# Performance work log

Hardware: AMD Instinct MI355X
Metric: run time of the kernel (lower is better)

The kernel has to match this reference:

```python
import jax, jax.numpy as jnp
import numpy as np

B, S, D = 4, 2048, 1024
H = 16
KD = 1024  # key_dim (total)
VD = 1024  # value_dim (total)


def setup_inputs() -> dict:
    key = jax.random.key(0)
    ks = jax.random.split(key, 8)
    queries = jax.random.normal(ks[0], (B, S, D), dtype=jnp.float32)
    keys_ = jax.random.normal(ks[1], (B, S, D), dtype=jnp.float32)
    values = jax.random.normal(ks[2], (B, S, D), dtype=jnp.float32)
    # causal float mask (1 = keep, 0 = masked), broadcasts over [B, H, S, S]
    mask = jnp.tril(jnp.ones((S, S), dtype=jnp.float32))[None, None]
    # Linear weights stored as [in, out] so forward is x @ W
    Wq = jax.random.normal(ks[3], (D, KD), dtype=jnp.float32) / np.sqrt(D)
    Wk = jax.random.normal(ks[4], (D, KD), dtype=jnp.float32) / np.sqrt(D)
    Wv = jax.random.normal(ks[5], (D, VD), dtype=jnp.float32) / np.sqrt(D)
    Wo = jax.random.normal(ks[6], (H * VD // H * H // H * 1 if False else VD, D), dtype=jnp.float32) / np.sqrt(VD)
    bo = jnp.zeros((D,), dtype=jnp.float32)
    return {"queries": queries, "keys": keys_, "values": values, "mask": mask,
            "Wq": Wq, "Wk": Wk, "Wv": Wv, "Wo": Wo, "bo": bo}


def reference(queries, keys, values, mask, Wq, Wk, Wv, Wo, bo):
    b, s, _ = queries.shape
    # project then split heads: [B, S, H, hd] -> [B, H, S, hd]
    q = (queries @ Wq).reshape(b, s, H, -1).transpose(0, 2, 1, 3)
    k = (keys @ Wk).reshape(b, s, H, -1).transpose(0, 2, 1, 3)
    v = (values @ Wv).reshape(b, s, H, -1).transpose(0, 2, 1, 3)
    dk = k.shape[-1]  # per-head key dim (scale uses post-split dk, as in source)
    logits = jnp.einsum('bhqd,bhkd->bhqk', q, k) / jnp.sqrt(jnp.float32(dk))
    logits = logits + (1.0 - mask) * (-1e9)
    attn = jax.nn.softmax(logits, axis=-1)  # dropout p=0 in eval -> identity
    o = jnp.einsum('bhqk,bhkd->bhqd', attn, v)
    o = o.transpose(0, 2, 1, 3).reshape(b, s, H * (VD // H))
    return o @ Wo + bo
```

## Files before the change

kernel.cpp:

```cpp
#include <hip/hip_runtime.h>
#include <hip/hip_bf16.h>

typedef __attribute__((ext_vector_type(8))) short s8v;
typedef __attribute__((ext_vector_type(4))) short s4v;
typedef __attribute__((ext_vector_type(4))) float f4v;

#define S_LEN 2048
#define NH 16
#define HD 64
#define DMODEL 1024
#define KVB 64
#define LOG2E 1.44269504088896f
#define FIXMAX 32.0f

__device__ __forceinline__ unsigned short f2bf(float f) {
  union { float f; unsigned int u; } v; v.f = f;
  return (unsigned short)((v.u + 0x7FFFu + ((v.u >> 16) & 1u)) >> 16);
}

__device__ __forceinline__ f4v mfma16(s8v a, s8v b, f4v c) {
  return __builtin_amdgcn_mfma_f32_16x16x32_bf16(a, b, c, 0, 0, 0);
}

__device__ __forceinline__ void gl_lds16(const unsigned short* g, unsigned short* l) {
  __builtin_amdgcn_global_load_lds(
      (const __attribute__((address_space(1))) void*)g,
      (__attribute__((address_space(3))) void*)l, 16, 0, 0);
}

__global__ __launch_bounds__(256)
void transpose_cast4(const float* __restrict__ w0, const float* __restrict__ w1,
                     const float* __restrict__ w2, const float* __restrict__ w3,
                     unsigned short* __restrict__ o0, unsigned short* __restrict__ o1,
                     unsigned short* __restrict__ o2, unsigned short* __restrict__ o3) {
  __shared__ float tile[32][33];
  const int z = blockIdx.z;
  const float* W = (z == 0) ? w0 : (z == 1) ? w1 : (z == 2) ? w2 : w3;
  unsigned short* Wt = (z == 0) ? o0 : (z == 1) ? o1 : (z == 2) ? o2 : o3;
  int x = threadIdx.x, y = threadIdx.y;
  int n0 = blockIdx.x * 32, k0 = blockIdx.y * 32;
#pragma unroll
  for (int i = 0; i < 32; i += 8)
    tile[y + i][x] = W[(size_t)(k0 + y + i) * DMODEL + n0 + x];
  __syncthreads();
#pragma unroll
  for (int i = 0; i < 32; i += 8)
    Wt[(size_t)(n0 + y + i) * DMODEL + k0 + x] = f2bf(tile[x][y + i]);
}

__global__ __launch_bounds__(256, 2)
void qkv_gemm(const float* __restrict__ Qf, const float* __restrict__ Kf,
              const float* __restrict__ Vf, const unsigned short* __restrict__ WqT,
              const unsigned short* __restrict__ WkT, const unsigned short* __restrict__ WvT,
              unsigned short* __restrict__ Qb, unsigned short* __restrict__ Kb,
              unsigned short* __restrict__ Vtb) {
  __shared__ unsigned short As[128 * 64];
  __shared__ unsigned short Bs[128 * 64];
  const int z = blockIdx.z;
  const float* Af = (z == 0) ? Qf : (z == 1) ? Kf : Vf;
  const unsigned short* Bt = (z == 0) ? WqT : (z == 1) ? WkT : WvT;
  unsigned short* C = (z == 0) ? Qb : (z == 1) ? Kb : Vtb;
  const float scale = (z == 0) ? 0.125f * LOG2E : 1.0f;

  const int t = threadIdx.x;
  const int l = t & 63;
  const int w = t >> 6, wr = w >> 1, wc = w & 1;
  const int m0 = blockIdx.x * 128, n0 = blockIdx.y * 128;
  const int lg = l >> 4, lm = l & 15;

  f4v acc[4][4];
#pragma unroll
  for (int i = 0; i < 4; i++)
#pragma unroll
    for (int j = 0; j < 4; j++) acc[i][j] = f4v{0.f, 0.f, 0.f, 0.f};

  const int lr = l >> 3;
  const int sj = l & 7;
  const float* Arow = Af + (size_t)(m0 + w * 8 + lr) * DMODEL + sj * 8;
  const unsigned short* Bprow =
      Bt + (size_t)(n0 + w * 8 + lr) * DMODEL + (sj ^ lr) * 8;
  const int xo0 = (lg ^ (lm & 7)) << 4;
  const int xo1 = ((4 + lg) ^ (lm & 7)) << 4;

  for (int k0 = 0; k0 < DMODEL; k0 += 64) {
#pragma unroll
    for (int i = 0; i < 4; i++)
      gl_lds16(Bprow + (size_t)(i * 32) * DMODEL + k0, &Bs[i * 2048 + w * 512]);
#pragma unroll
    for (int i = 0; i < 4; i++) {
      const float* src = Arow + (size_t)(i * 32) * DMODEL + k0;
      f4v v0 = *(const f4v*)src;
      f4v v1 = *(const f4v*)(src + 4);
      unsigned int u0, u1, u2, u3;
      asm("v_cvt_pk_bf16_f32 %0, %1, %2" : "=v"(u0) : "v"(v0[0]), "v"(v0[1]));
      asm("v_cvt_pk_bf16_f32 %0, %1, %2" : "=v"(u1) : "v"(v0[2]), "v"(v0[3]));
      asm("v_cvt_pk_bf16_f32 %0, %1, %2" : "=v"(u2) : "v"(v1[0]), "v"(v1[1]));
      asm("v_cvt_pk_bf16_f32 %0, %1, %2" : "=v"(u3) : "v"(v1[2]), "v"(v1[3]));
      uint4 pk; pk.x = u0; pk.y = u1; pk.z = u2; pk.w = u3;
      *(uint4*)((char*)As + (i * 32 + w * 8 + lr) * 128 + (sj ^ lr) * 16) = pk;
    }
    __syncthreads();

    s8v af[4][2], bf[4][2];
#pragma unroll
    for (int mi = 0; mi < 4; mi++) {
      const char* ar = (const char*)As + (wr * 64 + mi * 16 + lm) * 128;
      af[mi][0] = *(const s8v*)(ar + xo0);
      af[mi][1] = *(const s8v*)(ar + xo1);
    }
#pragma unroll
    for (int ni = 0; ni < 4; ni++) {
      const char* br = (const char*)Bs + (wc * 64 + ni * 16 + lm) * 128;
      bf[ni][0] = *(const s8v*)(br + xo0);
      bf[ni][1] = *(const s8v*)(br + xo1);
    }
#pragma unroll
    for (int mi = 0; mi < 4; mi++)
#pragma unroll
      for (int ni = 0; ni < 4; ni++) {
        acc[mi][ni] = mfma16(af[mi][0], bf[ni][0], acc[mi][ni]);
        acc[mi][ni] = mfma16(af[mi][1], bf[ni][1], acc[mi][ni]);
      }
    __syncthreads();
  }

#pragma unroll
  for (int mi = 0; mi < 4; mi++)
#pragma unroll
    for (int ni = 0; ni < 4; ni++) {
      int col = n0 + wc * 64 + ni * 16 + lm;
#pragma unroll
      for (int rr = 0; rr < 4; rr++) {
        int row = m0 + wr * 64 + mi * 16 + lg * 4 + rr;
        unsigned short h = f2bf(acc[mi][ni][rr] * scale);
        int b = row >> 11, s = row & 2047, hh = col >> 6, d = col & 63;
        if (z < 2)
          C[(((size_t)(b * NH + hh)) * S_LEN + s) * HD + d] = h;
        else
          C[(((size_t)(b * NH + hh)) * HD + d) * S_LEN + s] = h;
      }
    }
}

__global__ __launch_bounds__(256, 2)
void out_gemm(const unsigned short* __restrict__ A, const unsigned short* __restrict__ Bt,
              float* __restrict__ Cp, const float* __restrict__ bias) {
  __shared__ unsigned short As[128 * 64];
  __shared__ unsigned short Bs[128 * 64];
  const int t = threadIdx.x;
  const int l = t & 63;
  const int w = t >> 6, wr = w >> 1, wc = w & 1;
  const int m0 = blockIdx.x * 128, n0 = blockIdx.y * 128;
  const int lg = l >> 4, lm = l & 15;

  f4v acc[4][4];
#pragma unroll
  for (int i = 0; i < 4; i++)
#pragma unroll
    for (int j = 0; j < 4; j++) acc[i][j] = f4v{0.f, 0.f, 0.f, 0.f};

  const int sgc = (l & 7) ^ ((l >> 3) & 7);
  const unsigned short* Aprow = A + (size_t)(m0 + w * 8 + (l >> 3)) * DMODEL + sgc * 8;
  const unsigned short* Bprow = Bt + (size_t)(n0 + w * 8 + (l >> 3)) * DMODEL + sgc * 8;
  const int xo0 = (lg ^ (lm & 7)) << 4;
  const int xo1 = ((4 + lg) ^ (lm & 7)) << 4;

  for (int k0 = 0; k0 < DMODEL; k0 += 64) {
#pragma unroll
    for (int i = 0; i < 4; i++) {
      gl_lds16(Aprow + (size_t)(i * 32) * DMODEL + k0, &As[i * 2048 + w * 512]);
      gl_lds16(Bprow + (size_t)(i * 32) * DMODEL + k0, &Bs[i * 2048 + w * 512]);
    }
    __syncthreads();

    s8v af[4][2], bf[4][2];
#pragma unroll
    for (int mi = 0; mi < 4; mi++) {
      const char* ar = (const char*)As + (wr * 64 + mi * 16 + lm) * 128;
      af[mi][0] = *(const s8v*)(ar + xo0);
      af[mi][1] = *(const s8v*)(ar + xo1);
    }
#pragma unroll
    for (int ni = 0; ni < 4; ni++) {
      const char* br = (const char*)Bs + (wc * 64 + ni * 16 + lm) * 128;
      bf[ni][0] = *(const s8v*)(br + xo0);
      bf[ni][1] = *(const s8v*)(br + xo1);
    }
#pragma unroll
    for (int mi = 0; mi < 4; mi++)
#pragma unroll
      for (int ni = 0; ni < 4; ni++) {
        acc[mi][ni] = mfma16(af[mi][0], bf[ni][0], acc[mi][ni]);
        acc[mi][ni] = mfma16(af[mi][1], bf[ni][1], acc[mi][ni]);
      }
    __syncthreads();
  }

#pragma unroll
  for (int mi = 0; mi < 4; mi++)
#pragma unroll
    for (int ni = 0; ni < 4; ni++) {
      int col = n0 + wc * 64 + ni * 16 + lm;
      float bv = bias[col];
#pragma unroll
      for (int rr = 0; rr < 4; rr++) {
        int row = m0 + wr * 64 + mi * 16 + lg * 4 + rr;
        Cp[(size_t)row * DMODEL + col] = acc[mi][ni][rr] + bv;
      }
    }
}

__global__ __launch_bounds__(256, 2)
void attn_k(const unsigned short* __restrict__ Q, const unsigned short* __restrict__ Km,
            const unsigned short* __restrict__ Vt, unsigned short* __restrict__ O) {
  __shared__ unsigned short Ks[2][KVB * HD];
  __shared__ unsigned short Vs[2][HD * KVB];
  __shared__ unsigned short pbuf[16][16 * KVB];
  const int t = threadIdx.x, l = t & 63, w = t >> 6;
  const int lg = l >> 4, lm = l & 15;

  const int c = blockIdx.x;
  const int bh = c & 63;
  const int pr4 = (c >> 6) & 3;
  const int pr = (c >> 8) ? 7 - pr4 : pr4;
  const int s0A = (15 - pr) * 128, s0B = pr * 128;

  const unsigned short* Qh = Q + (size_t)bh * S_LEN * HD;
  const unsigned short* Kh = Km + (size_t)bh * S_LEN * HD;
  const unsigned short* Vh = Vt + (size_t)bh * HD * S_LEN;

  const int xo0 = (lg ^ (lm & 7)) << 4;
  const int xo1 = ((4 + lg) ^ (lm & 7)) << 4;

  const int q00 = s0A + w * 32, q01 = q00 + 16;
  const int q02 = s0B + w * 32, q03 = q02 + 16;

  s8v qf0[2], qf1[2], qf2[2], qf3[2];
#define LOADQ(QF, Q0)                                                   \
  QF[0] = *(const s8v*)(Qh + (size_t)((Q0) + lm) * HD + lg * 8);        \
  QF[1] = *(const s8v*)(Qh + (size_t)((Q0) + lm) * HD + 32 + lg * 8);
  LOADQ(qf0, q00) LOADQ(qf1, q01) LOADQ(qf2, q02) LOADQ(qf3, q03)
#undef LOADQ

  f4v o0[4], o1[4], o2[4], o3[4];
#pragma unroll
  for (int i = 0; i < 4; i++) {
    o0[i] = f4v{0.f, 0.f, 0.f, 0.f}; o1[i] = f4v{0.f, 0.f, 0.f, 0.f};
    o2[i] = f4v{0.f, 0.f, 0.f, 0.f}; o3[i] = f4v{0.f, 0.f, 0.f, 0.f};
  }
  float l0_ = 0.f, l1_ = 0.f, l2_ = 0.f, l3_ = 0.f;

  const int sr0 = w * 8 + (l >> 3);
  const int sj = l & 7;

#define STAGE(buf, kv)                                                          \
  {                                                                             \
    _Pragma("unroll")                                                           \
    for (int i = 0; i < 2; i++) {                                               \
      int r_ = sr0 + i * 32;                                                    \
      int jj_ = ((sj ^ (r_ & 7)) << 3);                                         \
      gl_lds16(Kh + (size_t)((kv) + r_) * HD + jj_, &Ks[buf][w * 512 + i * 2048]); \
      gl_lds16(Vh + (size_t)r_ * S_LEN + (kv) + jj_, &Vs[buf][w * 512 + i * 2048]); \
    }                                                                           \
  }

#define TILE_S(QF, LL, Q0, PI)                                                  \
  {                                                                             \
    const int dt = (Q0) >> 6;                                                   \
    if (ti <= dt) {                                                             \
      f4v s_[4];                                                                \
      __builtin_amdgcn_s_setprio(1);                                            \
      _Pragma("unroll")                                                         \
      for (int sub = 0; sub < 4; sub++) {                                       \
        s_[sub] = f4v{0.f, 0.f, 0.f, 0.f};                                      \
        s_[sub] = mfma16(kf[sub * 2], QF[0], s_[sub]);                          \
        s_[sub] = mfma16(kf[sub * 2 + 1], QF[1], s_[sub]);                      \
      }                                                                         \
      __builtin_amdgcn_s_setprio(0);                                            \
      if (ti == dt) {                                                           \
        const int qrow = (Q0) + lm;                                             \
        _Pragma("unroll")                                                       \
        for (int sub = 0; sub < 4; sub++) {                                     \
          const int kbase = kv + sub * 16 + lg * 4;                             \
          _Pragma("unroll")                                                     \
          for (int rr = 0; rr < 4; rr++)                                        \
            if (kbase + rr > qrow) s_[sub][rr] = -1e30f;                        \
        }                                                                       \
      }                                                                         \
      char* pb_ = (char*)pbuf[w * 4 + PI];                                      \
      float psum = 0.f;                                                         \
      _Pragma("unroll")                                                         \
      for (int sub = 0; sub < 4; sub++) {                                       \
        float p0 = exp2f(s_[sub][0] - FIXMAX);                                  \
        float p1 = exp2f(s_[sub][1] - FIXMAX);                                  \
        float p2 = exp2f(s_[sub][2] - FIXMAX);                                  \
        float p3 = exp2f(s_[sub][3] - FIXMAX);                                  \
        psum += (p0 + p1) + (p2 + p3);                                          \
        unsigned int u01, u23;                                                  \
        asm("v_cvt_pk_bf16_f32 %0, %1, %2" : "=v"(u01) : "v"(p0), "v"(p1));     \
        asm("v_cvt_pk_bf16_f32 %0, %1, %2" : "=v"(u23) : "v"(p2), "v"(p3));     \
        const int cc = (sub * 4 + lg) ^ ((lm & 7) << 1);                        \
        uint2 pv; pv.x = u01; pv.y = u23;                                       \
        *(uint2*)(pb_ + lm * 128 + (cc << 3)) = pv;                             \
      }                                                                         \
      (LL) += psum;                                                             \
    }                                                                           \
  }

#define TILE_PV(OO, Q0, PI)                                                     \
  {                                                                             \
    const int dt = (Q0) >> 6;                                                   \
    if (ti <= dt) {                                                             \
      const char* pb_ = (const char*)pbuf[w * 4 + PI];                          \
      s8v pf0 = *(const s8v*)(pb_ + lm * 128 + xo0);                            \
      s8v pf1 = *(const s8v*)(pb_ + lm * 128 + xo1);                            \
      __builtin_amdgcn_s_setprio(1);                                            \
      _Pragma("unroll")                                                         \
      for (int nc = 0; nc < 4; nc++) {                                          \
        OO[nc] = mfma16(vf[nc * 2], pf0, OO[nc]);                               \
        OO[nc] = mfma16(vf[nc * 2 + 1], pf1, OO[nc]);                           \
      }                                                                         \
      __builtin_amdgcn_s_setprio(0);                                            \
    }                                                                           \
  }

  const int nt = 2 * (15 - pr) + 2;
  int cur = 0;
  STAGE(0, 0);
  __syncthreads();

  for (int ti = 0; ti < nt; ++ti) {
    const int kv = ti * 64;
    if (ti + 1 < nt) STAGE(cur ^ 1, kv + 64);

    const unsigned short* Kb = Ks[cur];
    const unsigned short* Vb = Vs[cur];

    s8v kf[8];
#pragma unroll
    for (int sub = 0; sub < 4; sub++) {
      const char* krow = (const char*)Kb + (sub * 16 + lm) * 128;
      kf[sub * 2] = *(const s8v*)(krow + xo0);
      kf[sub * 2 + 1] = *(const s8v*)(krow + xo1);
    }

    TILE_S(qf0, l0_, q00, 0);
    TILE_S(qf1, l1_, q01, 1);
    TILE_S(qf2, l2_, q02, 2);
    TILE_S(qf3, l3_, q03, 3);

    __builtin_amdgcn_sched_barrier(0);

    s8v vf[8];
#pragma unroll
    for (int sub = 0; sub < 4; sub++) {
      const char* vrow = (const char*)Vb + (sub * 16 + lm) * 128;
      vf[sub * 2] = *(const s8v*)(vrow + xo0);
      vf[sub * 2 + 1] = *(const s8v*)(vrow + xo1);
    }

    TILE_PV(o0, q00, 0);
    TILE_PV(o1, q01, 1);
    TILE_PV(o2, q02, 2);
    TILE_PV(o3, q03, 3);

    __syncthreads();
    cur ^= 1;
  }

  const int b = bh >> 4, hh = bh & 15;
#define EPI(OO, LL, Q0)                                                         \
  {                                                                             \
    float lt = (LL);                                                            \
    lt += __shfl_xor(lt, 16);                                                   \
    lt += __shfl_xor(lt, 32);                                                   \
    const float inv = 1.f / lt;                                                 \
    unsigned short* Orow =                                                      \
        O + ((size_t)b * S_LEN + (Q0) + lm) * DMODEL + hh * HD;                 \
    _Pragma("unroll")                                                           \
    for (int nc = 0; nc < 4; nc++) {                                            \
      unsigned short h4[4];                                                     \
      _Pragma("unroll")                                                         \
      for (int rr = 0; rr < 4; rr++) h4[rr] = f2bf(OO[nc][rr] * inv);           \
      *(s4v*)(Orow + nc * 16 + lg * 4) = *(const s4v*)h4;                       \
    }                                                                           \
  }
  EPI(o0, l0_, q00);
  EPI(o1, l1_, q01);
  EPI(o2, l2_, q02);
  EPI(o3, l3_, q03);
#undef EPI
#undef TILE_PV
#undef TILE_S
#undef STAGE
}

extern "C" void kernel_launch(void* const* d_in, const int* in_sizes, int n_in,
                              void* d_out, int out_size, void* d_ws, size_t ws_size,
                              hipStream_t stream) {
  const float* queries = (const float*)d_in[0];
  const float* keys = (const float*)d_in[1];
  const float* values = (const float*)d_in[2];
  const float* Wq = (const float*)d_in[4];
  const float* Wk = (const float*)d_in[5];
  const float* Wv = (const float*)d_in[6];
  const float* Wo = (const float*)d_in[7];
  const float* bo = (const float*)d_in[8];

  char* ws = (char*)d_ws;
  const size_t WB = (size_t)DMODEL * DMODEL * 2;
  unsigned short* WqT = (unsigned short*)(ws + 0 * WB);
  unsigned short* WkT = (unsigned short*)(ws + 1 * WB);
  unsigned short* WvT = (unsigned short*)(ws + 2 * WB);
  unsigned short* WoT = (unsigned short*)(ws + 3 * WB);
  const size_t TB = (size_t)4 * S_LEN * DMODEL * 2;
  unsigned short* Qb  = (unsigned short*)(ws + 4 * WB);
  unsigned short* Kb  = (unsigned short*)(ws + 4 * WB + TB);
  unsigned short* Vtb = (unsigned short*)(ws + 4 * WB + 2 * TB);
  unsigned short* Ob  = (unsigned short*)(ws + 4 * WB + 3 * TB);

  const int M = 4 * S_LEN;

  transpose_cast4<<<dim3(32, 32, 4), dim3(32, 8), 0, stream>>>(
      Wq, Wk, Wv, Wo, WqT, WkT, WvT, WoT);

  qkv_gemm<<<dim3(64, 8, 3), 256, 0, stream>>>(queries, keys, values,
                                               WqT, WkT, WvT, Qb, Kb, Vtb);

  attn_k<<<512, 256, 0, stream>>>(Qb, Kb, Vtb, Ob);

  out_gemm<<<dim3(64, 8), 256, 0, stream>>>(Ob, WoT, (float*)d_out, bo);
}
```

Measured before the change: 176.9 us.

## Double-buffer LDS tiles in QKV projection GEMM to overlap loads with MFMA

Doubles the shared-memory A and B tiles in the QKV projection GEMM. The next k-slice is loaded (async B copy plus A fp32-to-bf16 convert and store) while the current slice is read and fed to MFMA, leaving one barrier per iteration instead of two. This hides global-load latency behind compute. In exchange, LDS use doubles to 64KB per block, which may lower occupancy against the launch bound of 2 blocks per CU.

Result: slower. 201.7 us (+14.0%).

```diff
diff --git a/kernel.cpp b/kernel.cpp
--- a/kernel.cpp
+++ b/kernel.cpp
@@ -54,8 +54,8 @@
               const unsigned short* __restrict__ WkT, const unsigned short* __restrict__ WvT,
               unsigned short* __restrict__ Qb, unsigned short* __restrict__ Kb,
               unsigned short* __restrict__ Vtb) {
-  __shared__ unsigned short As[128 * 64];
-  __shared__ unsigned short Bs[128 * 64];
+  __shared__ unsigned short As[2][128 * 64];
+  __shared__ unsigned short Bs[2][128 * 64];
   const int z = blockIdx.z;
   const float* Af = (z == 0) ? Qf : (z == 1) ? Kf : Vf;
   const unsigned short* Bt = (z == 0) ? WqT : (z == 1) ? WkT : WvT;
@@ -82,38 +82,55 @@
   const int xo0 = (lg ^ (lm & 7)) << 4;
   const int xo1 = ((4 + lg) ^ (lm & 7)) << 4;
 
+#define STAGE_A(bb, kk)                                                         \
+  {                                                                             \
+    _Pragma("unroll")                                                           \
+    for (int i = 0; i < 4; i++) {                                               \
+      const float* src = Arow + (size_t)(i * 32) * DMODEL + (kk);               \
+      f4v v0 = *(const f4v*)src;                                                \
+      f4v v1 = *(const f4v*)(src + 4);                                          \
+      unsigned int u0, u1, u2, u3;                                              \
+      asm("v_cvt_pk_bf16_f32 %0, %1, %2" : "=v"(u0) : "v"(v0[0]), "v"(v0[1]));  \
+      asm("v_cvt_pk_bf16_f32 %0, %1, %2" : "=v"(u1) : "v"(v0[2]), "v"(v0[3]));  \
+      asm("v_cvt_pk_bf16_f32 %0, %1, %2" : "=v"(u2) : "v"(v1[0]), "v"(v1[1]));  \
+      asm("v_cvt_pk_bf16_f32 %0, %1, %2" : "=v"(u3) : "v"(v1[2]), "v"(v1[3]));  \
+      uint4 pk; pk.x = u0; pk.y = u1; pk.z = u2; pk.w = u3;                     \
+      *(uint4*)((char*)As[bb] + (i * 32 + w * 8 + lr) * 128 + (sj ^ lr) * 16) = pk; \
+    }                                                                           \
+  }
+#define STAGE_B(bb, kk)                                                         \
+  {                                                                             \
+    _Pragma("unroll")                                                           \
+    for (int i = 0; i < 4; i++)                                                 \
+      gl_lds16(Bprow + (size_t)(i * 32) * DMODEL + (kk),                        \
+               &Bs[bb][i * 2048 + w * 512]);                                    \
+  }
+
+  STAGE_B(0, 0);
+  STAGE_A(0, 0);
+  __syncthreads();
+  int cur = 0;
+
   for (int k0 = 0; k0 < DMODEL; k0 += 64) {
-#pragma unroll
-    for (int i = 0; i < 4; i++)
-      gl_lds16(Bprow + (size_t)(i * 32) * DMODEL + k0, &Bs[i * 2048 + w * 512]);
-#pragma unroll
-    for (int i = 0; i < 4; i++) {
-      const float* src = Arow + (size_t)(i * 32) * DMODEL + k0;
-      f4v v0 = *(const f4v*)src;
-      f4v v1 = *(const f4v*)(src + 4);
-      unsigned int u0, u1, u2, u3;
-      asm("v_cvt_pk_bf16_f32 %0, %1, %2" : "=v"(u0) : "v"(v0[0]), "v"(v0[1]));
-      asm("v_cvt_pk_bf16_f32 %0, %1, %2" : "=v"(u1) : "v"(v0[2]), "v"(v0[3]));
-      asm("v_cvt_pk_bf16_f32 %0, %1, %2" : "=v"(u2) : "v"(v1[0]), "v"(v1[1]));
-      asm("v_cvt_pk_bf16_f32 %0, %1, %2" : "=v"(u3) : "v"(v1[2]), "v"(v1[3]));
-      uint4 pk; pk.x = u0; pk.y = u1; pk.z = u2; pk.w = u3;
-      *(uint4*)((char*)As + (i * 32 + w * 8 + lr) * 128 + (sj ^ lr) * 16) = pk;
-    }
-    __syncthreads();
+    const bool more = (k0 + 64 < DMODEL);
+    if (more) STAGE_B(cur ^ 1, k0 + 64);
 
     s8v af[4][2], bf[4][2];
 #pragma unroll
     for (int mi = 0; mi < 4; mi++) {
-      const char* ar = (const char*)As + (wr * 64 + mi * 16 + lm) * 128;
+      const char* ar = (const char*)As[cur] + (wr * 64 + mi * 16 + lm) * 128;
       af[mi][0] = *(const s8v*)(ar + xo0);
       af[mi][1] = *(const s8v*)(ar + xo1);
     }
 #pragma unroll
     for (int ni = 0; ni < 4; ni++) {
-      const char* br = (const char*)Bs + (wc * 64 + ni * 16 + lm) * 128;
+      const char* br = (const char*)Bs[cur] + (wc * 64 + ni * 16 + lm) * 128;
       bf[ni][0] = *(const s8v*)(br + xo0);
       bf[ni][1] = *(const s8v*)(br + xo1);
     }
+
+    if (more) STAGE_A(cur ^ 1, k0 + 64);
+
 #pragma unroll
     for (int mi = 0; mi < 4; mi++)
 #pragma unroll
@@ -122,7 +139,10 @@
         acc[mi][ni] = mfma16(af[mi][1], bf[ni][1], acc[mi][ni]);
       }
     __syncthreads();
-  }
+    cur ^= 1;
+  }
+#undef STAGE_A
+#undef STAGE_B
 
 #pragma unroll
   for (int mi = 0; mi < 4; mi++)
```
